# Kernel optimization log

Hardware: AMD Instinct MI355X
Metric: run time of the kernel (lower is better)

The kernel has to match this reference:

```python
import jax, jax.numpy as jnp
import numpy as np

ALPHA = 0.2  # LeakyReLU negative slope
NEG_BIG = -9e15


def setup_inputs() -> dict:
    key = jax.random.key(0)
    k1, k2, k3, k4 = jax.random.split(key, 4)
    N, F_in, F_out = 8192, 512, 256
    h = jax.random.normal(k1, (N, F_in), dtype=jnp.float32)
    adj = jax.random.randint(k2, (N, N), 0, 2, dtype=jnp.int32)
    # xavier_uniform with gain=1.414
    lim_W = 1.414 * np.sqrt(6.0 / (F_in + F_out))
    W = jax.random.uniform(k3, (F_in, F_out), jnp.float32, -lim_W, lim_W)
    lim_a = 1.414 * np.sqrt(6.0 / (2 * F_out + 1))
    a = jax.random.uniform(k4, (2 * F_out, 1), jnp.float32, -lim_a, lim_a)
    return {"h": h, "adj": adj, "W": W, "a": a}


def reference(h, adj, W, a):
    # Wh: [N, F_out]
    Wh = h @ W
    F_out = Wh.shape[1]
    # Decomposed score: e_ij = leakyrelu(a1.Wh_i + a2.Wh_j)
    f1 = Wh @ a[:F_out, 0]   # [N]
    f2 = Wh @ a[F_out:, 0]   # [N]
    e = f1[:, None] + f2[None, :]          # [N, N]
    e = jax.nn.leaky_relu(e, ALPHA)
    e = jnp.where(adj > 0, e, NEG_BIG)
    attention = jax.nn.softmax(e, axis=1)  # dropout omitted (eval mode)
    h_prime = attention @ Wh               # [N, F_out]
    return jax.nn.elu(h_prime)             # concat=True
```

## Files before the change

### kernel.cpp

```cpp
#include <hip/hip_runtime.h>
#include <hip/hip_bf16.h>
#include <cstdint>

#define NV 8192
#define FIN 512
#define FOUT 256
#define KS 4
#define ALPHA_LRELU 0.2f

using bf16x8 = __attribute__((ext_vector_type(8))) short;
using f32x4  = __attribute__((ext_vector_type(4))) float;

static __device__ __forceinline__ float b2f(ushort u) {
  union { uint32_t u32; float f; } v; v.u32 = ((uint32_t)u) << 16; return v.f;
}
static __device__ __forceinline__ ushort f2b(float f) {
  union { float f; uint32_t u; } v; v.f = f;
  uint32_t r = (v.u + 0x7fffu + ((v.u >> 16) & 1u)) >> 16;
  return (ushort)r;
}
static __device__ __forceinline__ uint32_t pk2(float a, float b) {
  return (uint32_t)f2b(a) | ((uint32_t)f2b(b) << 16);
}
static __device__ __forceinline__ int swz(int row, int kchunk) {
  return (row << 6) + (((kchunk ^ (row & 7)) & 7) << 3);
}
static __device__ __forceinline__ void gl_lds16(const ushort* g, ushort* l) {
  __builtin_amdgcn_global_load_lds(
      (const __attribute__((address_space(1))) uint32_t*)(uintptr_t)g,
      (__attribute__((address_space(3))) uint32_t*)(uint32_t)(uintptr_t)l,
      16, 0, 0);
}
#define SBAR0() __builtin_amdgcn_sched_barrier(0)

__global__ void k_prep_w(const float* __restrict__ W, ushort* __restrict__ WT,
                         float* __restrict__ f1z) {
  int t = blockIdx.x * 256 + threadIdx.x;
  int n = t >> 9, k = t & 511;
  WT[(size_t)n * FIN + k] = f2b(W[(size_t)k * FOUT + n]);
  if (t < 2 * NV) f1z[t] = 0.f;
}

__global__ __launch_bounds__(256, 4) void k_gemm1(
    const float* __restrict__ h, const ushort* __restrict__ WT,
    const float* __restrict__ a,
    ushort* __restrict__ WhT, float* __restrict__ f1, float* __restrict__ f2) {
  __shared__ __align__(16) ushort As[64 * 64];
  __shared__ __align__(16) ushort Ws[64 * 64];
  const int t = threadIdx.x;
  const int lane = t & 63;
  const int w = t >> 6;
  const int wm = w >> 1, wn = w & 1;
  const int i0 = blockIdx.x * 64;
  const int n0 = blockIdx.y * 64;

  f32x4 acc[2][2] = {};
  const int srow = t & 63, sseg = t >> 6;

  for (int kt = 0; kt < FIN / 64; ++kt) {
    const int k0 = kt * 64;
    {
      const float4* gA = (const float4*)(h + (size_t)(i0 + srow) * FIN + k0 + sseg * 16);
      float4 v0 = gA[0], v1 = gA[1], v2 = gA[2], v3 = gA[3];
      uint4 c0, c1;
      c0.x = pk2(v0.x, v0.y); c0.y = pk2(v0.z, v0.w);
      c0.z = pk2(v1.x, v1.y); c0.w = pk2(v1.z, v1.w);
      c1.x = pk2(v2.x, v2.y); c1.y = pk2(v2.z, v2.w);
      c1.z = pk2(v3.x, v3.y); c1.w = pk2(v3.z, v3.w);
      *(uint4*)&As[swz(srow, sseg * 2 + 0)] = c0;
      *(uint4*)&As[swz(srow, sseg * 2 + 1)] = c1;
    }
    {
      const uint4* gB = (const uint4*)(WT + (size_t)(n0 + srow) * FIN + k0 + sseg * 16);
      uint4 b0 = gB[0], b1 = gB[1];
      *(uint4*)&Ws[swz(srow, sseg * 2 + 0)] = b0;
      *(uint4*)&Ws[swz(srow, sseg * 2 + 1)] = b1;
    }
    __syncthreads();
#pragma unroll
    for (int kk = 0; kk < 2; ++kk) {
      const int kc = kk * 4 + (lane >> 4);
      bf16x8 af[2], bfv[2];
#pragma unroll
      for (int fi = 0; fi < 2; ++fi)
        af[fi] = *(const bf16x8*)&As[swz(wm * 32 + fi * 16 + (lane & 15), kc)];
#pragma unroll
      for (int fj = 0; fj < 2; ++fj)
        bfv[fj] = *(const bf16x8*)&Ws[swz(wn * 32 + fj * 16 + (lane & 15), kc)];
#pragma unroll
      for (int fi = 0; fi < 2; ++fi)
#pragma unroll
        for (int fj = 0; fj < 2; ++fj)
          acc[fi][fj] = __builtin_amdgcn_mfma_f32_16x16x32_bf16(af[fi], bfv[fj], acc[fi][fj], 0, 0, 0);
    }
    __syncthreads();
  }

  float p1[2][4] = {}, p2[2][4] = {};
#pragma unroll
  for (int fi = 0; fi < 2; ++fi) {
    const int row0 = i0 + wm * 32 + fi * 16 + ((lane >> 4) << 2);
#pragma unroll
    for (int fj = 0; fj < 2; ++fj) {
      const int col = n0 + wn * 32 + fj * 16 + (lane & 15);
      const float a1c = a[col], a2c = a[FOUT + col];
      ushort ov[4];
      ushort4 o;
#pragma unroll
      for (int rr = 0; rr < 4; ++rr) {
        ov[rr] = f2b(acc[fi][fj][rr]);
        float v = b2f(ov[rr]);
        p1[fi][rr] = fmaf(v, a1c, p1[fi][rr]);
        p2[fi][rr] = fmaf(v, a2c, p2[fi][rr]);
      }
      o.x = ov[0]; o.y = ov[1]; o.z = ov[2]; o.w = ov[3];
      *(ushort4*)&WhT[(size_t)col * NV + row0] = o;
    }
  }
#pragma unroll
  for (int fi = 0; fi < 2; ++fi)
#pragma unroll
    for (int rr = 0; rr < 4; ++rr) {
      float s1 = p1[fi][rr], s2 = p2[fi][rr];
#pragma unroll
      for (int m = 1; m < 16; m <<= 1) {
        s1 += __shfl_xor(s1, m);
        s2 += __shfl_xor(s2, m);
      }
      if ((lane & 15) == 0) {
        const int row = i0 + wm * 32 + fi * 16 + ((lane >> 4) << 2) + rr;
        atomicAdd(&f1[row], s1);
        atomicAdd(&f2[row], s2);
      }
    }
}

__global__ __launch_bounds__(512, 4) void k_gemm2(
    const int* __restrict__ adj, const ushort* __restrict__ WhT,
    const float* __restrict__ f1, const float* __restrict__ f2,
    float* __restrict__ accP, float* __restrict__ Sp) {
  __shared__ __align__(16) ushort Ps[2][64 * 64];
  __shared__ __align__(16) ushort Bs[2][256 * 64];

  const int t = threadIdx.x;
  const int lane = t & 63;
  const int w = t >> 6;
  const int wm = w >> 2, wn = w & 3;
  const int bid = blockIdx.x;
  const int ks = bid & (KS - 1);
  const int rb = bid >> 2;
  const int i0 = rb * 64;
  const int jbase = ks * (NV / KS);
  const int NT = (NV / KS) / 64;

  const int pr = t >> 3, pq = t & 7;
  const float f1r = f1[i0 + pr];

  const int lrow = lane >> 3;
  const int lchunk = (lane & 7) ^ lrow;
  const ushort* wsrc0 = WhT + (size_t)(w * 32 + lrow) * NV + jbase + lchunk * 8;
  const int* adjp = adj + (size_t)(i0 + pr) * NV + jbase + pq * 8;
  const float* f2p = f2 + jbase + pq * 8;

  float ssum = 0.f;
  f32x4 acc[2][4] = {};
  int avA[8], avB[8];
  float fzA[8], fzB[8];

  auto adjload = [&](int tile, int (&av)[8]) {
    int4 a0 = *(const int4*)(adjp + tile * 64);
    int4 a1 = *(const int4*)(adjp + tile * 64 + 4);
    av[0] = a0.x; av[1] = a0.y; av[2] = a0.z; av[3] = a0.w;
    av[4] = a1.x; av[5] = a1.y; av[6] = a1.z; av[7] = a1.w;
  };
  auto fzload = [&](int tile, float (&fz)[8]) {
    float4 z0 = *(const float4*)(f2p + tile * 64);
    float4 z1 = *(const float4*)(f2p + tile * 64 + 4);
    fz[0] = z0.x; fz[1] = z0.y; fz[2] = z0.z; fz[3] = z0.w;
    fz[4] = z1.x; fz[5] = z1.y; fz[6] = z1.z; fz[7] = z1.w;
  };
  auto glB = [&](int tile, int buf) {
    const int koff = tile * 64;
#pragma unroll
    for (int q = 0; q < 4; ++q)
      gl_lds16(wsrc0 + (size_t)q * 8 * NV + koff, &Bs[buf][(w * 4 + q) * 512]);
  };
  auto finish = [&](const int (&av)[8], const float (&fz)[8], int buf) {
    ushort ub[8];
#pragma unroll
    for (int e = 0; e < 8; ++e) {
      float x = f1r + fz[e];
      float ee = fminf(fmaxf(x, ALPHA_LRELU * x), 75.f);
      float wv = (av[e] > 0) ? __expf(ee) : 0.f;
      ub[e] = f2b(wv);
      ssum += b2f(ub[e]);
    }
    uint4 pk;
    pk.x = (uint32_t)ub[0] | ((uint32_t)ub[1] << 16);
    pk.y = (uint32_t)ub[2] | ((uint32_t)ub[3] << 16);
    pk.z = (uint32_t)ub[4] | ((uint32_t)ub[5] << 16);
    pk.w = (uint32_t)ub[6] | ((uint32_t)ub[7] << 16);
    *(uint4*)&Ps[buf][swz(pr, pq)] = pk;
  };
  auto mfma_step = [&](int buf) {
#pragma unroll
    for (int kk = 0; kk < 2; ++kk) {
      const int kc = kk * 4 + (lane >> 4);
      bf16x8 af[2], bfv[4];
#pragma unroll
      for (int fi = 0; fi < 2; ++fi)
        af[fi] = *(const bf16x8*)&Ps[buf][swz(wm * 32 + fi * 16 + (lane & 15), kc)];
#pragma unroll
      for (int fj = 0; fj < 4; ++fj)
        bfv[fj] = *(const bf16x8*)&Bs[buf][swz(wn * 64 + fj * 16 + (lane & 15), kc)];
#pragma unroll
      for (int fi = 0; fi < 2; ++fi)
#pragma unroll
        for (int fj = 0; fj < 4; ++fj)
          acc[fi][fj] = __builtin_amdgcn_mfma_f32_16x16x32_bf16(af[fi], bfv[fj], acc[fi][fj], 0, 0, 0);
    }
  };

  glB(0, 0);
  adjload(0, avA); fzload(0, fzA);
  adjload(1, avB); fzload(1, fzB);
  SBAR0();
  finish(avA, fzA, 0);
  __syncthreads();

  for (int kt = 0; kt + 2 < NT; kt += 2) {
    glB(kt + 1, 1);
    adjload(kt + 2, avA); fzload(kt + 2, fzA);
    SBAR0();
    finish(avB, fzB, 1);
    mfma_step(0);
    __syncthreads();
    glB(kt + 2, 0);
    adjload(kt + 3, avB); fzload(kt + 3, fzB);
    SBAR0();
    finish(avA, fzA, 0);
    mfma_step(1);
    __syncthreads();
  }

  glB(NT - 1, 1);
  SBAR0();
  finish(avB, fzB, 1);
  mfma_step(0);
  __syncthreads();
  mfma_step(1);

  ssum += __shfl_xor(ssum, 1);
  ssum += __shfl_xor(ssum, 2);
  ssum += __shfl_xor(ssum, 4);
  if (pq == 0) Sp[(size_t)ks * NV + i0 + pr] = ssum;

  float* ab = accP + (size_t)ks * NV * FOUT;
#pragma unroll
  for (int fi = 0; fi < 2; ++fi) {
    const int ig = i0 + wm * 32 + fi * 16 + ((lane >> 4) << 2);
#pragma unroll
    for (int fj = 0; fj < 4; ++fj) {
      const int col = wn * 64 + fj * 16 + (lane & 15);
#pragma unroll
      for (int rr = 0; rr < 4; ++rr)
        ab[(size_t)(ig + rr) * FOUT + col] = acc[fi][fj][rr];
    }
  }
}

__global__ void k_combine(const float* __restrict__ accP, const float* __restrict__ Sp,
                          float* __restrict__ out) {
  const size_t NF = (size_t)NV * FOUT;
  int g = blockIdx.x * 256 + threadIdx.x;
  int i = g >> 6;
  float4 v0 = ((const float4*)accP)[g];
  float4 v1 = ((const float4*)(accP + NF))[g];
  float4 v2 = ((const float4*)(accP + 2 * NF))[g];
  float4 v3 = ((const float4*)(accP + 3 * NF))[g];
  float s = Sp[i] + Sp[NV + i] + Sp[2 * NV + i] + Sp[3 * NV + i];
  float inv = (s != 0.f) ? (1.0f / s) : 0.f;
  float xs0 = (v0.x + v1.x + v2.x + v3.x) * inv;
  float xs1 = (v0.y + v1.y + v2.y + v3.y) * inv;
  float xs2 = (v0.z + v1.z + v2.z + v3.z) * inv;
  float xs3 = (v0.w + v1.w + v2.w + v3.w) * inv;
  float4 o;
  o.x = xs0 > 0.f ? xs0 : expm1f(xs0);
  o.y = xs1 > 0.f ? xs1 : expm1f(xs1);
  o.z = xs2 > 0.f ? xs2 : expm1f(xs2);
  o.w = xs3 > 0.f ? xs3 : expm1f(xs3);
  ((float4*)out)[g] = o;
}

extern "C" void kernel_launch(void* const* d_in, const int* in_sizes, int n_in,
                              void* d_out, int out_size, void* d_ws, size_t ws_size,
                              hipStream_t stream) {
  const float* h   = (const float*)d_in[0];
  const int*   adj = (const int*)d_in[1];
  const float* W   = (const float*)d_in[2];
  const float* a   = (const float*)d_in[3];
  float* out = (float*)d_out;

  char* ws = (char*)d_ws;
  ushort* WT   = (ushort*)ws;
  ushort* WhT  = (ushort*)(ws + (256ull << 10));
  float*  f1   = (float*)(ws + (256ull << 10) + (4ull << 20));
  float*  f2   = f1 + NV;
  float*  Sp   = f2 + NV;
  float*  accP = Sp + (size_t)KS * NV;

  k_prep_w<<<(FIN * FOUT) / 256, 256, 0, stream>>>(W, WT, f1);
  k_gemm1<<<dim3(NV / 64, FOUT / 64), 256, 0, stream>>>(h, WT, a, WhT, f1, f2);
  k_gemm2<<<(NV / 64) * KS, 512, 0, stream>>>(adj, WhT, f1, f2, accP, Sp);
  k_combine<<<(NV * FOUT / 4) / 256, 256, 0, stream>>>(accP, Sp, out);
}
```

Before: 425.2 us.

## Double-buffer gemm1 LDS tiles and issue MFMA before softmax finish in attention kernel

The first GEMM (h@W) now uses double-buffered LDS with register prefetch of the next two k-tiles, so global loads and the fp32-to-bf16 conversion overlap MFMA work. Its occupancy hint drops from 4 to 2 blocks per CU to make room for the extra registers and LDS. In the main attention kernel, the MFMA step is moved ahead of the finish stage (adjacency/score exponent computation) within each half-iteration, so matrix work can overlap that vector work. The risk is higher register pressure and lower occupancy in gemm1.

```diff
diff --git a/kernel.cpp b/kernel.cpp
--- a/kernel.cpp
+++ b/kernel.cpp
@@ -41,60 +41,82 @@
   if (t < 2 * NV) f1z[t] = 0.f;
 }
 
-__global__ __launch_bounds__(256, 4) void k_gemm1(
+__global__ __launch_bounds__(256, 2) void k_gemm1(
     const float* __restrict__ h, const ushort* __restrict__ WT,
     const float* __restrict__ a,
     ushort* __restrict__ WhT, float* __restrict__ f1, float* __restrict__ f2) {
-  __shared__ __align__(16) ushort As[64 * 64];
-  __shared__ __align__(16) ushort Ws[64 * 64];
+  __shared__ __align__(16) ushort As[2][64 * 64];
+  __shared__ __align__(16) ushort Ws[2][64 * 64];
   const int t = threadIdx.x;
   const int lane = t & 63;
   const int w = t >> 6;
   const int wm = w >> 1, wn = w & 1;
   const int i0 = blockIdx.x * 64;
   const int n0 = blockIdx.y * 64;
+  const int srow = t & 63, sseg = t >> 6;
+  const int NT1 = FIN / 64;
 
   f32x4 acc[2][2] = {};
-  const int srow = t & 63, sseg = t >> 6;
-
-  for (int kt = 0; kt < FIN / 64; ++kt) {
-    const int k0 = kt * 64;
-    {
-      const float4* gA = (const float4*)(h + (size_t)(i0 + srow) * FIN + k0 + sseg * 16);
-      float4 v0 = gA[0], v1 = gA[1], v2 = gA[2], v3 = gA[3];
-      uint4 c0, c1;
-      c0.x = pk2(v0.x, v0.y); c0.y = pk2(v0.z, v0.w);
-      c0.z = pk2(v1.x, v1.y); c0.w = pk2(v1.z, v1.w);
-      c1.x = pk2(v2.x, v2.y); c1.y = pk2(v2.z, v2.w);
-      c1.z = pk2(v3.x, v3.y); c1.w = pk2(v3.z, v3.w);
-      *(uint4*)&As[swz(srow, sseg * 2 + 0)] = c0;
-      *(uint4*)&As[swz(srow, sseg * 2 + 1)] = c1;
-    }
-    {
-      const uint4* gB = (const uint4*)(WT + (size_t)(n0 + srow) * FIN + k0 + sseg * 16);
-      uint4 b0 = gB[0], b1 = gB[1];
-      *(uint4*)&Ws[swz(srow, sseg * 2 + 0)] = b0;
-      *(uint4*)&Ws[swz(srow, sseg * 2 + 1)] = b1;
-    }
-    __syncthreads();
+  uint4 hA0, hA1, wA0, wA1;
+  uint4 hB0, hB1, wB0, wB1;
+
+  auto loadregs = [&](int kt, uint4& h0, uint4& h1, uint4& w0, uint4& w1) {
+    const float4* gA = (const float4*)(h + (size_t)(i0 + srow) * FIN + kt * 64 + sseg * 16);
+    float4 v0 = gA[0], v1 = gA[1], v2 = gA[2], v3 = gA[3];
+    h0.x = pk2(v0.x, v0.y); h0.y = pk2(v0.z, v0.w);
+    h0.z = pk2(v1.x, v1.y); h0.w = pk2(v1.z, v1.w);
+    h1.x = pk2(v2.x, v2.y); h1.y = pk2(v2.z, v2.w);
+    h1.z = pk2(v3.x, v3.y); h1.w = pk2(v3.z, v3.w);
+    const uint4* gB = (const uint4*)(WT + (size_t)(n0 + srow) * FIN + kt * 64 + sseg * 16);
+    w0 = gB[0]; w1 = gB[1];
+  };
+  auto writeLds = [&](const uint4& h0, const uint4& h1, const uint4& w0, const uint4& w1,
+                      int buf) {
+    *(uint4*)&As[buf][swz(srow, sseg * 2 + 0)] = h0;
+    *(uint4*)&As[buf][swz(srow, sseg * 2 + 1)] = h1;
+    *(uint4*)&Ws[buf][swz(srow, sseg * 2 + 0)] = w0;
+    *(uint4*)&Ws[buf][swz(srow, sseg * 2 + 1)] = w1;
+  };
+  auto mfma1 = [&](int buf) {
 #pragma unroll
     for (int kk = 0; kk < 2; ++kk) {
       const int kc = kk * 4 + (lane >> 4);
       bf16x8 af[2], bfv[2];
 #pragma unroll
       for (int fi = 0; fi < 2; ++fi)
-        af[fi] = *(const bf16x8*)&As[swz(wm * 32 + fi * 16 + (lane & 15), kc)];
+        af[fi] = *(const bf16x8*)&As[buf][swz(wm * 32 + fi * 16 + (lane & 15), kc)];
 #pragma unroll
       for (int fj = 0; fj < 2; ++fj)
-        bfv[fj] = *(const bf16x8*)&Ws[swz(wn * 32 + fj * 16 + (lane & 15), kc)];
+        bfv[fj] = *(const bf16x8*)&Ws[buf][swz(wn * 32 + fj * 16 + (lane & 15), kc)];
 #pragma unroll
       for (int fi = 0; fi < 2; ++fi)
 #pragma unroll
         for (int fj = 0; fj < 2; ++fj)
           acc[fi][fj] = __builtin_amdgcn_mfma_f32_16x16x32_bf16(af[fi], bfv[fj], acc[fi][fj], 0, 0, 0);
     }
+  };
+
+  loadregs(0, hA0, hA1, wA0, wA1);
+  loadregs(1, hB0, hB1, wB0, wB1);
+  writeLds(hA0, hA1, wA0, wA1, 0);
+  __syncthreads();
+
+  for (int kt = 0; kt + 2 < NT1; kt += 2) {
+    loadregs(kt + 2, hA0, hA1, wA0, wA1);
+    SBAR0();
+    mfma1(0);
+    writeLds(hB0, hB1, wB0, wB1, 1);
+    __syncthreads();
+    loadregs(kt + 3, hB0, hB1, wB0, wB1);
+    SBAR0();
+    mfma1(1);
+    writeLds(hA0, hA1, wA0, wA1, 0);
     __syncthreads();
   }
+  mfma1(0);
+  writeLds(hB0, hB1, wB0, wB1, 1);
+  __syncthreads();
+  mfma1(1);
 
   float p1[2][4] = {}, p2[2][4] = {};
 #pragma unroll
@@ -232,21 +254,21 @@
     glB(kt + 1, 1);
     adjload(kt + 2, avA); fzload(kt + 2, fzA);
     SBAR0();
+    mfma_step(0);
     finish(avB, fzB, 1);
-    mfma_step(0);
     __syncthreads();
     glB(kt + 2, 0);
     adjload(kt + 3, avB); fzload(kt + 3, fzB);
     SBAR0();
+    mfma_step(1);
     finish(avA, fzA, 0);
-    mfma_step(1);
     __syncthreads();
   }
 
   glB(NT - 1, 1);
   SBAR0();
+  mfma_step(0);
   finish(avB, fzB, 1);
-  mfma_step(0);
   __syncthreads();
   mfma_step(1);
 
```

New measurement: 423.6 us. No clear change (-0.4%).
